# Kernel optimization log

Measured on AMD Instinct MI355X. Metric: run time of the kernel, lower is better.

## Reference

```python
import jax, jax.numpy as jnp
import numpy as np

B, S, D, H = 8, 1024, 1024, 16
HD = D // H
EPS = 1e-06


def setup_inputs() -> dict:
    key = jax.random.key(0)
    ks = jax.random.split(key, 10)
    sc = 0.02
    inp = {
        "y": jax.random.normal(ks[0], (B, S, D), dtype=jnp.float32),
        "y_mask": jax.random.randint(ks[1], (B, 1, 1, S), 0, 2) == 1,
        "Wq": jax.random.normal(ks[2], (D, D), dtype=jnp.float32) * sc,
        "bq": jnp.zeros((D,), jnp.float32),
        "Wk": jax.random.normal(ks[3], (D, D), dtype=jnp.float32) * sc,
        "bk": jnp.zeros((D,), jnp.float32),
        "Wv": jax.random.normal(ks[4], (D, D), dtype=jnp.float32) * sc,
        "bv": jnp.zeros((D,), jnp.float32),
        "Wm": jax.random.normal(ks[5], (D, D), dtype=jnp.float32) * sc,
        "bm": jnp.zeros((D,), jnp.float32),
        "a2": jnp.ones((D,), jnp.float32),
        "b2": jnp.zeros((D,), jnp.float32),
    }
    return inp


def _heads(x):
    # [B,S,D] -> [B,H,S,HD]
    return x.reshape(B, S, H, HD).transpose(0, 2, 1, 3)


def reference(y, y_mask, Wq, bq, Wk, bk, Wv, bv, Wm, bm, a2, b2):
    # torch Linear: x @ W^T + b
    q = _heads(y @ Wq.T + bq)
    k = _heads(y @ Wk.T + bk)
    v = _heads(y @ Wv.T + bv)
    scores = jnp.einsum("bhqd,bhkd->bhqk", q, k) / jnp.sqrt(jnp.float32(HD))
    scores = jnp.where(y_mask, jnp.float32(-1e9), scores)
    att = jax.nn.softmax(scores, axis=-1)  # dropout = identity in eval
    atted = jnp.einsum("bhqk,bhkd->bhqd", att, v)
    atted = atted.transpose(0, 2, 1, 3).reshape(B, S, D)
    atted = atted @ Wm.T + bm
    x = y + atted  # residual (dropout1 = identity in eval)
    mean = x.mean(-1, keepdims=True)
    # torch std: unbiased (ddof=1); eps added to std, not variance
    std = jnp.sqrt(((x - mean) ** 2).sum(-1, keepdims=True) / jnp.float32(D - 1))
    return a2 * (x - mean) / (std + EPS) + b2
```

## Files before the change

### kernel.cpp

```cpp
#include <hip/hip_runtime.h>

#define DEVFN __device__ __forceinline__

typedef unsigned short u16;
typedef __attribute__((ext_vector_type(8))) unsigned short u16x8;
typedef __attribute__((ext_vector_type(4))) unsigned short u16x4;
typedef __attribute__((ext_vector_type(8))) __bf16 bf16x8;
typedef __attribute__((ext_vector_type(4))) float f32x4;

DEVFN u16 f2bf(float f) {
    unsigned u = __builtin_bit_cast(unsigned, f);
    u += 0x7FFFu + ((u >> 16) & 1u);
    return (u16)(u >> 16);
}

DEVFN u16 f2bf_hw(float f) {
    return __builtin_bit_cast(u16, (__bf16)f);
}

DEVFN bf16x8 ldfrag(const u16* p) {
    return __builtin_bit_cast(bf16x8, *(const u16x8*)p);
}

DEVFN f32x4 mfma16(bf16x8 a, bf16x8 b, f32x4 c) {
    return __builtin_amdgcn_mfma_f32_16x16x32_bf16(a, b, c, 0, 0, 0);
}

DEVFN void async16(const u16* g, u16* l) {
    __builtin_amdgcn_global_load_lds(
        (const __attribute__((address_space(1))) void*)g,
        (__attribute__((address_space(3))) void*)l, 16, 0, 0);
}

__global__ __launch_bounds__(256) void to_bf16(const float* __restrict__ in,
                                               u16* __restrict__ outp, int n) {
    const int i = (blockIdx.x * 256 + threadIdx.x) * 4;
    if (i >= n) return;
    const float4 v = *(const float4*)&in[i];
    u16x4 o;
    o.x = f2bf(v.x); o.y = f2bf(v.y); o.z = f2bf(v.z); o.w = f2bf(v.w);
    *(u16x4*)&outp[i] = o;
}

template <bool BF16OUT>
__global__ __launch_bounds__(256) void gemm_bt(const u16* __restrict__ A,
                                               const u16* __restrict__ Bt,
                                               const float* __restrict__ b0,
                                               const float* __restrict__ b1,
                                               const float* __restrict__ b2,
                                               void* __restrict__ C0,
                                               void* __restrict__ C1,
                                               void* __restrict__ C2,
                                               int K) {
    __shared__ u16 lA[128 * 32];
    __shared__ u16 lB[128 * 32];
    const int tid = threadIdx.x;
    const int wave = tid >> 6, lane = tid & 63;
    const int quad = lane >> 4, l16 = lane & 15;
    const int m0 = blockIdx.y * 128, n0 = blockIdx.x * 128;
    const int wm = (wave >> 1) * 64, wn = (wave & 1) * 64;
    const int srow = tid >> 2, scol = (tid & 3) * 8;
    const u16* Ag0 = A + (size_t)(m0 + srow) * K + scol;
    const u16* Ag1 = A + (size_t)(m0 + 64 + srow) * K + scol;
    const u16* Bg0 = Bt + (size_t)(n0 + srow) * K + scol;
    const u16* Bg1 = Bt + (size_t)(n0 + 64 + srow) * K + scol;
    u16* lA0 = &lA[wave * 512];
    u16* lA1 = &lA[2048 + wave * 512];
    u16* lB0 = &lB[wave * 512];
    u16* lB1 = &lB[2048 + wave * 512];
    f32x4 acc[4][4] = {};
    for (int k0 = 0; k0 < K; k0 += 32) {
        __syncthreads();
        async16(Ag0 + k0, lA0);
        async16(Ag1 + k0, lA1);
        async16(Bg0 + k0, lB0);
        async16(Bg1 + k0, lB1);
        __syncthreads();
        bf16x8 af[4], bfr[4];
        #pragma unroll
        for (int i = 0; i < 4; ++i)
            af[i] = ldfrag(&lA[(wm + i * 16 + l16) * 32 + quad * 8]);
        #pragma unroll
        for (int i = 0; i < 4; ++i)
            bfr[i] = ldfrag(&lB[(wn + i * 16 + l16) * 32 + quad * 8]);
        #pragma unroll
        for (int mi = 0; mi < 4; ++mi)
            #pragma unroll
            for (int ni = 0; ni < 4; ++ni)
                acc[mi][ni] = mfma16(af[mi], bfr[ni], acc[mi][ni]);
    }
    #pragma unroll
    for (int mi = 0; mi < 4; ++mi) {
        #pragma unroll
        for (int ni = 0; ni < 4; ++ni) {
            const int col = n0 + wn + ni * 16 + l16;
            const int cs = col >> 10;
            const int c = col & 1023;
            const float* bp = cs == 0 ? b0 : (cs == 1 ? b1 : b2);
            void* cpv = cs == 0 ? C0 : (cs == 1 ? C1 : C2);
            const float bb = bp[c];
            #pragma unroll
            for (int r = 0; r < 4; ++r) {
                const int row = m0 + wm + mi * 16 + quad * 4 + r;
                const float v = acc[mi][ni][r] + bb;
                if constexpr (BF16OUT)
                    ((u16*)cpv)[(size_t)row * 1024 + c] = f2bf(v);
                else
                    ((float*)cpv)[(size_t)row * 1024 + c] = v;
            }
        }
    }
}

__global__ __launch_bounds__(256) void transpose_v(const u16* __restrict__ v,
                                                   u16* __restrict__ vt) {
    const int bh = blockIdx.y, bb = bh >> 4, h = bh & 15;
    const int s0 = blockIdx.x * 64;
    __shared__ u16 t[64 * 72];
    const int r = threadIdx.x >> 3, c8 = (threadIdx.x & 7) * 8;
    #pragma unroll
    for (int rr = 0; rr < 64; rr += 32)
        *(u16x8*)&t[(r + rr) * 72 + c8] =
            *(const u16x8*)&v[(size_t)(bb * 1024 + s0 + r + rr) * 1024 + h * 64 + c8];
    __syncthreads();
    #pragma unroll
    for (int rr = 0; rr < 64; rr += 32) {
        u16x8 o;
        #pragma unroll
        for (int j = 0; j < 8; ++j) o[j] = t[(c8 + j) * 72 + (r + rr)];
        *(u16x8*)&vt[(size_t)(bh * 64 + r + rr) * 1024 + s0 + c8] = o;
    }
}

__global__ __launch_bounds__(256) void attn(const u16* __restrict__ qb,
                                            const u16* __restrict__ kb,
                                            const u16* __restrict__ vtb,
                                            const int* __restrict__ mask,
                                            u16* __restrict__ attb) {
    const int lin = blockIdx.x + (blockIdx.y << 4);
    const int xcd = lin & 7, slot = lin >> 3;
    const int bh = xcd * 16 + (slot >> 4);
    const int q0 = (slot & 15) * 64;
    const int bb = bh >> 4, h = bh & 15;
    const int tid = threadIdx.x, wave = tid >> 6, lane = tid & 63;
    const int quad = lane >> 4, l16 = lane & 15;
    __shared__ u16 lK[64 * 72];
    __shared__ u16 lV[64 * 72];
    __shared__ u16 lP[4 * 16 * 72];
    __shared__ float lM[1024];

    const int* mrow = mask + bb * 1024;
    for (int i = tid; i < 1024; i += 256) lM[i] = mrow[i] ? -1e9f : 0.0f;

    const int qrow = q0 + wave * 16 + l16;
    const u16* qp = qb + (size_t)(bb * 1024 + qrow) * 1024 + h * 64 + quad * 8;
    const bf16x8 aq0 = ldfrag(qp);
    const bf16x8 aq1 = ldfrag(qp + 32);

    f32x4 o[4] = {};
    float ps_acc[4] = {0.f, 0.f, 0.f, 0.f};

    const int srow = tid >> 3, scol = (tid & 7) * 8;
    const u16* kbase = kb + (size_t)(bb * 1024) * 1024 + h * 64 + scol;
    const u16* vbase = vtb + (size_t)(bh * 64 + srow) * 1024 + scol;

    u16x8 nk0 = *(const u16x8*)(kbase + (size_t)srow * 1024);
    u16x8 nk1 = *(const u16x8*)(kbase + (size_t)(srow + 32) * 1024);
    u16x8 nv0 = *(const u16x8*)(vbase);
    u16x8 nv1 = *(const u16x8*)(vbase + (size_t)32 * 1024);

    for (int kt = 0; kt < 1024; kt += 64) {
        __syncthreads();
        *(u16x8*)&lK[srow * 72 + scol] = nk0;
        *(u16x8*)&lK[(srow + 32) * 72 + scol] = nk1;
        *(u16x8*)&lV[srow * 72 + scol] = nv0;
        *(u16x8*)&lV[(srow + 32) * 72 + scol] = nv1;
        __syncthreads();
        const int ktn = kt + 64;
        if (ktn < 1024) {
            nk0 = *(const u16x8*)(kbase + (size_t)(ktn + srow) * 1024);
            nk1 = *(const u16x8*)(kbase + (size_t)(ktn + srow + 32) * 1024);
            nv0 = *(const u16x8*)(vbase + ktn);
            nv1 = *(const u16x8*)(vbase + (size_t)32 * 1024 + ktn);
        }

        f32x4 s[4];
        #pragma unroll
        for (int n = 0; n < 4; ++n) {
            f32x4 t = {};
            t = mfma16(aq0, ldfrag(&lK[(n * 16 + l16) * 72 + quad * 8]), t);
            t = mfma16(aq1, ldfrag(&lK[(n * 16 + l16) * 72 + 32 + quad * 8]), t);
            s[n] = t;
        }
        #pragma unroll
        for (int n = 0; n < 4; ++n) {
            const float bias = lM[kt + n * 16 + l16];
            #pragma unroll
            for (int r = 0; r < 4; ++r) {
                const float p = __expf(s[n][r] * 0.125f + bias);
                ps_acc[r] += p;
                lP[(wave * 16 + quad * 4 + r) * 72 + n * 16 + l16] = f2bf_hw(p);
            }
        }
        __asm__ __volatile__("s_waitcnt lgkmcnt(0)" ::: "memory");
        const bf16x8 ap0 = ldfrag(&lP[(wave * 16 + l16) * 72 + quad * 8]);
        const bf16x8 ap1 = ldfrag(&lP[(wave * 16 + l16) * 72 + 32 + quad * 8]);
        #pragma unroll
        for (int ni = 0; ni < 4; ++ni) {
            o[ni] = mfma16(ap0, ldfrag(&lV[(ni * 16 + l16) * 72 + quad * 8]), o[ni]);
            o[ni] = mfma16(ap1, ldfrag(&lV[(ni * 16 + l16) * 72 + 32 + quad * 8]), o[ni]);
        }
    }
    #pragma unroll
    for (int off = 1; off < 16; off <<= 1)
        #pragma unroll
        for (int r = 0; r < 4; ++r)
            ps_acc[r] += __shfl_xor(ps_acc[r], off);
    float rl[4];
    #pragma unroll
    for (int r = 0; r < 4; ++r) rl[r] = 1.f / ps_acc[r];
    #pragma unroll
    for (int ni = 0; ni < 4; ++ni)
        #pragma unroll
        for (int r = 0; r < 4; ++r) {
            const int row = q0 + wave * 16 + quad * 4 + r;
            attb[(size_t)(bb * 1024 + row) * 1024 + h * 64 + ni * 16 + l16] =
                f2bf_hw(o[ni][r] * rl[r]);
        }
}

__global__ __launch_bounds__(256) void ln_res(const float* __restrict__ y,
                                              const float* __restrict__ xp,
                                              const float* __restrict__ a2,
                                              const float* __restrict__ b2,
                                              float* __restrict__ out) {
    const int row = blockIdx.x, tid = threadIdx.x;
    const size_t base = (size_t)row * 1024;
    const int j = tid * 4;
    const float4 yv = *(const float4*)&y[base + j];
    const float4 xv = *(const float4*)&xp[base + j];
    float x[4] = {yv.x + xv.x, yv.y + xv.y, yv.z + xv.z, yv.w + xv.w};
    float s = 0.f, ss = 0.f;
    #pragma unroll
    for (int i = 0; i < 4; ++i) { s += x[i]; ss += x[i] * x[i]; }
    #pragma unroll
    for (int off = 1; off < 64; off <<= 1) {
        s += __shfl_xor(s, off);
        ss += __shfl_xor(ss, off);
    }
    __shared__ float rs[4], rss[4];
    const int wave = tid >> 6, lane = tid & 63;
    if (lane == 0) { rs[wave] = s; rss[wave] = ss; }
    __syncthreads();
    s = rs[0] + rs[1] + rs[2] + rs[3];
    ss = rss[0] + rss[1] + rss[2] + rss[3];
    const float mean = s * (1.f / 1024.f);
    float var = (ss - s * mean) * (1.f / 1023.f);
    var = fmaxf(var, 0.f);
    const float inv = 1.f / (sqrtf(var) + 1e-6f);
    const float4 av = *(const float4*)&a2[j];
    const float4 bv = *(const float4*)&b2[j];
    float4 ov;
    ov.x = av.x * (x[0] - mean) * inv + bv.x;
    ov.y = av.y * (x[1] - mean) * inv + bv.y;
    ov.z = av.z * (x[2] - mean) * inv + bv.z;
    ov.w = av.w * (x[3] - mean) * inv + bv.w;
    *(float4*)&out[base + j] = ov;
}

extern "C" void kernel_launch(void* const* d_in, const int* in_sizes, int n_in,
                              void* d_out, int out_size, void* d_ws, size_t ws_size,
                              hipStream_t stream) {
    (void)in_sizes; (void)n_in; (void)out_size;
    const float* y   = (const float*)d_in[0];
    const int*   msk = (const int*)d_in[1];
    const float* Wq  = (const float*)d_in[2];
    const float* bq  = (const float*)d_in[3];
    const float* Wk  = (const float*)d_in[4];
    const float* bkb = (const float*)d_in[5];
    const float* Wv  = (const float*)d_in[6];
    const float* bv  = (const float*)d_in[7];
    const float* Wm  = (const float*)d_in[8];
    const float* bm  = (const float*)d_in[9];
    const float* a2  = (const float*)d_in[10];
    const float* b2  = (const float*)d_in[11];
    float* out = (float*)d_out;

    char* ws = (char*)d_ws;
    const size_t MB = 1u << 20;
    if (ws_size < 72 * MB) return;
    u16* yb  = (u16*)(ws);
    u16* wqb = (u16*)(ws + 16 * MB);
    u16* wkb = (u16*)(ws + 18 * MB);
    u16* wvb = (u16*)(ws + 20 * MB);
    u16* wmb = (u16*)(ws + 22 * MB);
    u16* qb  = (u16*)(ws + 24 * MB);
    u16* kb  = (u16*)(ws + 40 * MB);
    u16* vb  = (u16*)(ws + 56 * MB);
    u16* vtb  = yb;
    u16* attb = vb;
    float* xp = (float*)(ws + 24 * MB);

    const int MT = 8192;
    to_bf16<<<MT * 1024 / 1024, 256, 0, stream>>>(y, yb, MT * 1024);
    to_bf16<<<1024, 256, 0, stream>>>(Wq, wqb, 1024 * 1024);
    to_bf16<<<1024, 256, 0, stream>>>(Wk, wkb, 1024 * 1024);
    to_bf16<<<1024, 256, 0, stream>>>(Wv, wvb, 1024 * 1024);
    to_bf16<<<1024, 256, 0, stream>>>(Wm, wmb, 1024 * 1024);

    gemm_bt<true><<<dim3(24, 64), 256, 0, stream>>>(
        yb, wqb, bq, bkb, bv, qb, kb, vb, 1024);

    transpose_v<<<dim3(16, 128), 256, 0, stream>>>(vb, vtb);
    attn<<<dim3(16, 128), 256, 0, stream>>>(qb, kb, vtb, msk, attb);

    gemm_bt<false><<<dim3(8, 64), 256, 0, stream>>>(
        attb, wmb, bm, bm, bm, xp, xp, xp, 1024);
    ln_res<<<MT, 256, 0, stream>>>(y, xp, a2, b2, out);
}
```

Before: 314.8 us.

## Double attention query tile per block and merge weight conversion launches

The attention kernel now processes 128 query rows per block, two 16-row groups per wave, so each K/V tile loaded into shared memory is reused across twice as many queries. The block count halves to 1024 on a 1D grid. The softmax exponent becomes exp2 with a prescaled fma, and the four weight-to-bf16 conversions are merged into one launch. This cuts K/V global traffic and launch overhead, at the cost of more registers per thread and fewer blocks, which may lower occupancy.

```diff
diff --git a/kernel.cpp b/kernel.cpp
--- a/kernel.cpp
+++ b/kernel.cpp
@@ -40,6 +40,20 @@
     u16x4 o;
     o.x = f2bf(v.x); o.y = f2bf(v.y); o.z = f2bf(v.z); o.w = f2bf(v.w);
     *(u16x4*)&outp[i] = o;
+}
+
+__global__ __launch_bounds__(256) void w4_to_bf16(const float* __restrict__ w0,
+                                                  const float* __restrict__ w1,
+                                                  const float* __restrict__ w2,
+                                                  const float* __restrict__ w3,
+                                                  u16* __restrict__ outp) {
+    const int g = blockIdx.y;
+    const float* in = g == 0 ? w0 : (g == 1 ? w1 : (g == 2 ? w2 : w3));
+    const int i = (blockIdx.x * 256 + threadIdx.x) * 4;
+    const float4 v = *(const float4*)&in[i];
+    u16x4 o;
+    o.x = f2bf(v.x); o.y = f2bf(v.y); o.z = f2bf(v.z); o.w = f2bf(v.w);
+    *(u16x4*)&outp[(size_t)g * 1024 * 1024 + i] = o;
 }
 
 template <bool BF16OUT>
@@ -137,28 +151,32 @@
                                             const u16* __restrict__ vtb,
                                             const int* __restrict__ mask,
                                             u16* __restrict__ attb) {
-    const int lin = blockIdx.x + (blockIdx.y << 4);
+    const int lin = blockIdx.x;
     const int xcd = lin & 7, slot = lin >> 3;
-    const int bh = xcd * 16 + (slot >> 4);
-    const int q0 = (slot & 15) * 64;
+    const int bh = xcd * 16 + (slot >> 3);
+    const int q0 = (slot & 7) * 128;
     const int bb = bh >> 4, h = bh & 15;
     const int tid = threadIdx.x, wave = tid >> 6, lane = tid & 63;
     const int quad = lane >> 4, l16 = lane & 15;
     __shared__ u16 lK[64 * 72];
     __shared__ u16 lV[64 * 72];
-    __shared__ u16 lP[4 * 16 * 72];
+    __shared__ u16 lP[128 * 72];
     __shared__ float lM[1024];
 
     const int* mrow = mask + bb * 1024;
     for (int i = tid; i < 1024; i += 256) lM[i] = mrow[i] ? -1e9f : 0.0f;
 
-    const int qrow = q0 + wave * 16 + l16;
-    const u16* qp = qb + (size_t)(bb * 1024 + qrow) * 1024 + h * 64 + quad * 8;
-    const bf16x8 aq0 = ldfrag(qp);
-    const bf16x8 aq1 = ldfrag(qp + 32);
-
-    f32x4 o[4] = {};
-    float ps_acc[4] = {0.f, 0.f, 0.f, 0.f};
+    bf16x8 aq[2][2];
+    #pragma unroll
+    for (int rg = 0; rg < 2; ++rg) {
+        const int qrow = q0 + wave * 32 + rg * 16 + l16;
+        const u16* qp = qb + (size_t)(bb * 1024 + qrow) * 1024 + h * 64 + quad * 8;
+        aq[rg][0] = ldfrag(qp);
+        aq[rg][1] = ldfrag(qp + 32);
+    }
+
+    f32x4 o[2][4] = {};
+    float ps_acc[2][4] = {};
 
     const int srow = tid >> 3, scol = (tid & 7) * 8;
     const u16* kbase = kb + (size_t)(bb * 1024) * 1024 + h * 64 + scol;
@@ -168,6 +186,8 @@
     u16x8 nk1 = *(const u16x8*)(kbase + (size_t)(srow + 32) * 1024);
     u16x8 nv0 = *(const u16x8*)(vbase);
     u16x8 nv1 = *(const u16x8*)(vbase + (size_t)32 * 1024);
+
+    const float C = 0.18033688011112043f;
 
     for (int kt = 0; kt < 1024; kt += 64) {
         __syncthreads();
@@ -184,49 +204,80 @@
             nv1 = *(const u16x8*)(vbase + (size_t)32 * 1024 + ktn);
         }
 
-        f32x4 s[4];
+        bf16x8 kf[4][2];
         #pragma unroll
         for (int n = 0; n < 4; ++n) {
-            f32x4 t = {};
-            t = mfma16(aq0, ldfrag(&lK[(n * 16 + l16) * 72 + quad * 8]), t);
-            t = mfma16(aq1, ldfrag(&lK[(n * 16 + l16) * 72 + 32 + quad * 8]), t);
-            s[n] = t;
-        }
-        #pragma unroll
-        for (int n = 0; n < 4; ++n) {
-            const float bias = lM[kt + n * 16 + l16];
+            kf[n][0] = ldfrag(&lK[(n * 16 + l16) * 72 + quad * 8]);
+            kf[n][1] = ldfrag(&lK[(n * 16 + l16) * 72 + 32 + quad * 8]);
+        }
+        f32x4 s[2][4];
+        #pragma unroll
+        for (int rg = 0; rg < 2; ++rg)
+            #pragma unroll
+            for (int n = 0; n < 4; ++n) {
+                f32x4 t = {};
+                t = mfma16(aq[rg][0], kf[n][0], t);
+                t = mfma16(aq[rg][1], kf[n][1], t);
+                s[rg][n] = t;
+            }
+        float bias[4];
+        #pragma unroll
+        for (int n = 0; n < 4; ++n) bias[n] = lM[kt + n * 16 + l16];
+        #pragma unroll
+        for (int rg = 0; rg < 2; ++rg)
+            #pragma unroll
+            for (int n = 0; n < 4; ++n)
+                #pragma unroll
+                for (int r = 0; r < 4; ++r) {
+                    const float p =
+                        __builtin_amdgcn_exp2f(__builtin_fmaf(s[rg][n][r], C, bias[n]));
+                    ps_acc[rg][r] += p;
+                    lP[(wave * 32 + rg * 16 + quad * 4 + r) * 72 + n * 16 + l16] =
+                        f2bf_hw(p);
+                }
+        __asm__ __volatile__("s_waitcnt lgkmcnt(0)" ::: "memory");
+        bf16x8 ap[2][2];
+        #pragma unroll
+        for (int rg = 0; rg < 2; ++rg) {
+            ap[rg][0] = ldfrag(&lP[(wave * 32 + rg * 16 + l16) * 72 + quad * 8]);
+            ap[rg][1] = ldfrag(&lP[(wave * 32 + rg * 16 + l16) * 72 + 32 + quad * 8]);
+        }
+        bf16x8 vf[4][2];
+        #pragma unroll
+        for (int ni = 0; ni < 4; ++ni) {
+            vf[ni][0] = ldfrag(&lV[(ni * 16 + l16) * 72 + quad * 8]);
+            vf[ni][1] = ldfrag(&lV[(ni * 16 + l16) * 72 + 32 + quad * 8]);
+        }
+        #pragma unroll
+        for (int rg = 0; rg < 2; ++rg)
+            #pragma unroll
+            for (int ni = 0; ni < 4; ++ni) {
+                o[rg][ni] = mfma16(ap[rg][0], vf[ni][0], o[rg][ni]);
+                o[rg][ni] = mfma16(ap[rg][1], vf[ni][1], o[rg][ni]);
+            }
+    }
+    #pragma unroll
+    for (int off = 1; off < 16; off <<= 1)
+        #pragma unroll
+        for (int rg = 0; rg < 2; ++rg)
+            #pragma unroll
+            for (int r = 0; r < 4; ++r)
+                ps_acc[rg][r] += __shfl_xor(ps_acc[rg][r], off);
+    float rl[2][4];
+    #pragma unroll
+    for (int rg = 0; rg < 2; ++rg)
+        #pragma unroll
+        for (int r = 0; r < 4; ++r) rl[rg][r] = 1.f / ps_acc[rg][r];
+    #pragma unroll
+    for (int rg = 0; rg < 2; ++rg)
+        #pragma unroll
+        for (int ni = 0; ni < 4; ++ni)
             #pragma unroll
             for (int r = 0; r < 4; ++r) {
-                const float p = __expf(s[n][r] * 0.125f + bias);
-                ps_acc[r] += p;
-                lP[(wave * 16 + quad * 4 + r) * 72 + n * 16 + l16] = f2bf_hw(p);
+                const int row = q0 + wave * 32 + rg * 16 + quad * 4 + r;
+                attb[(size_t)(bb * 1024 + row) * 1024 + h * 64 + ni * 16 + l16] =
+                    f2bf_hw(o[rg][ni][r] * rl[rg][r]);
             }
-        }
-        __asm__ __volatile__("s_waitcnt lgkmcnt(0)" ::: "memory");
-        const bf16x8 ap0 = ldfrag(&lP[(wave * 16 + l16) * 72 + quad * 8]);
-        const bf16x8 ap1 = ldfrag(&lP[(wave * 16 + l16) * 72 + 32 + quad * 8]);
-        #pragma unroll
-        for (int ni = 0; ni < 4; ++ni) {
-            o[ni] = mfma16(ap0, ldfrag(&lV[(ni * 16 + l16) * 72 + quad * 8]), o[ni]);
-            o[ni] = mfma16(ap1, ldfrag(&lV[(ni * 16 + l16) * 72 + 32 + quad * 8]), o[ni]);
-        }
-    }
-    #pragma unroll
-    for (int off = 1; off < 16; off <<= 1)
-        #pragma unroll
-        for (int r = 0; r < 4; ++r)
-            ps_acc[r] += __shfl_xor(ps_acc[r], off);
-    float rl[4];
-    #pragma unroll
-    for (int r = 0; r < 4; ++r) rl[r] = 1.f / ps_acc[r];
-    #pragma unroll
-    for (int ni = 0; ni < 4; ++ni)
-        #pragma unroll
-        for (int r = 0; r < 4; ++r) {
-            const int row = q0 + wave * 16 + quad * 4 + r;
-            attb[(size_t)(bb * 1024 + row) * 1024 + h * 64 + ni * 16 + l16] =
-                f2bf_hw(o[ni][r] * rl[r]);
-        }
 }
 
 __global__ __launch_bounds__(256) void ln_res(const float* __restrict__ y,
@@ -291,8 +342,6 @@
     if (ws_size < 72 * MB) return;
     u16* yb  = (u16*)(ws);
     u16* wqb = (u16*)(ws + 16 * MB);
-    u16* wkb = (u16*)(ws + 18 * MB);
-    u16* wvb = (u16*)(ws + 20 * MB);
     u16* wmb = (u16*)(ws + 22 * MB);
     u16* qb  = (u16*)(ws + 24 * MB);
     u16* kb  = (u16*)(ws + 40 * MB);
@@ -303,16 +352,13 @@
 
     const int MT = 8192;
     to_bf16<<<MT * 1024 / 1024, 256, 0, stream>>>(y, yb, MT * 1024);
-    to_bf16<<<1024, 256, 0, stream>>>(Wq, wqb, 1024 * 1024);
-    to_bf16<<<1024, 256, 0, stream>>>(Wk, wkb, 1024 * 1024);
-    to_bf16<<<1024, 256, 0, stream>>>(Wv, wvb, 1024 * 1024);
-    to_bf16<<<1024, 256, 0, stream>>>(Wm, wmb, 1024 * 1024);
+    w4_to_bf16<<<dim3(1024, 4), 256, 0, stream>>>(Wq, Wk, Wv, Wm, wqb);
 
     gemm_bt<true><<<dim3(24, 64), 256, 0, stream>>>(
         yb, wqb, bq, bkb, bv, qb, kb, vb, 1024);
 
     transpose_v<<<dim3(16, 128), 256, 0, stream>>>(vb, vtb);
-    attn<<<dim3(16, 128), 256, 0, stream>>>(qb, kb, vtb, msk, attb);
+    attn<<<dim3(1024), 256, 0, stream>>>(qb, kb, vtb, msk, attb);
 
     gemm_bt<false><<<dim3(8, 64), 256, 0, stream>>>(
         attb, wmb, bm, bm, bm, xp, xp, xp, 1024);
```

After: 298.8 us. 5.1% less time.
